# Optimization experiments

Hardware: AMD Instinct MI355X
Metric: run time of the kernel (lower is better)

Reference implementation:

```python
import jax, jax.numpy as jnp
import numpy as np

E, H, W = 1024, 16, 256  # embed_dim, num_heads, window_size
D = E // H               # head_dim


def _rmsnorm(t, w):
    eps = jnp.finfo(t.dtype).eps
    return t * jax.lax.rsqrt(jnp.mean(t * t, axis=-1, keepdims=True) + eps) * w


def setup_inputs() -> dict:
    key = jax.random.key(0)
    ks = jax.random.split(key, 11)
    B, T = 2, 2048
    s = 1.0 / np.sqrt(E)
    return {
        "x": jax.random.normal(ks[0], (B, T, E), jnp.float32),
        "wq": jax.random.normal(ks[1], (E, E), jnp.float32) * s,
        "bq": jnp.zeros((E,), jnp.float32),
        "wk": jax.random.normal(ks[2], (E, E), jnp.float32) * s,
        "bk": jnp.zeros((E,), jnp.float32),
        "wv": jax.random.normal(ks[3], (E, E), jnp.float32) * s,
        "bv": jnp.zeros((E,), jnp.float32),
        "wo": jax.random.normal(ks[4], (E, E), jnp.float32) * s,
        "bo": jnp.zeros((E,), jnp.float32),
        "qn_w": jnp.ones((D,), jnp.float32),
        "kn_w": jnp.ones((D,), jnp.float32),
    }


def reference(x, wq, bq, wk, bk, wv, bv, wo, bo, qn_w, kn_w):
    B, T, _ = x.shape
    # projections; weights stored (in, out)
    q = (x @ wq + bq).reshape(B, T, H, D).transpose(0, 2, 1, 3)  # [B,H,T,D]
    k = (x @ wk + bk).reshape(B, T, H, D).transpose(0, 2, 1, 3)
    v = (x @ wv + bv).reshape(B, T, H, D).transpose(0, 2, 1, 3)
    q = _rmsnorm(q, qn_w)
    k = _rmsnorm(k, kn_w)

    scores = jnp.einsum("bhqd,bhkd->bhqk", q, k) / jnp.sqrt(jnp.float32(D))
    row = jnp.arange(T)[:, None]
    col = jnp.arange(T)[None, :]
    invalid = (col > row) | (row - col >= W)  # causal + sliding window
    neg_inf = jnp.float32(-jnp.inf)
    scores = jnp.where(invalid, neg_inf, scores)

    # genetic fitness reweighting
    masked_attn = jnp.where(invalid, 0.0, jax.nn.softmax(scores, axis=-1))
    gene_means = jnp.mean(jax.nn.sigmoid(masked_attn), axis=-1)  # [B,H,T]
    denom = gene_means + 0.5
    sum_inv = jnp.sum(1.0 / denom, axis=2, keepdims=True)        # [B,H,1]
    fitness = 1.0 / (denom * sum_inv)                            # [B,H,T]
    scores = scores + jnp.log(fitness)[..., None]

    attn = jax.nn.softmax(scores, axis=-1)
    out = jnp.einsum("bhqk,bhkd->bhqd", attn, v)
    out = out.transpose(0, 2, 1, 3).reshape(B, T, E)
    return out @ wo + bo
```

## Files before the change

### kernel.cpp

```cpp
#include <hip/hip_runtime.h>

typedef _Float16 f16;
typedef _Float16 f16x4 __attribute__((ext_vector_type(4)));
typedef _Float16 f16x8 __attribute__((ext_vector_type(8)));
typedef float f32x4 __attribute__((ext_vector_type(4)));

#define MFMA16(a, b, c) __builtin_amdgcn_mfma_f32_16x16x32_f16(a, b, c, 0, 0, 0)

constexpr int T = 2048;
constexpr int E = 1024;
constexpr int H = 16;
constexpr int D = 64;
constexpr int WIN = 256;
#define NEGF (-1e30f)
#define L2E 1.4426950408889634f

__device__ __forceinline__ void gload16(const f16* g, f16* l) {
  __builtin_amdgcn_global_load_lds(
      (__attribute__((address_space(1))) void*)(void*)g,
      (__attribute__((address_space(3))) void*)(void*)l, 16, 0, 0);
}

__global__ __launch_bounds__(256) void cast_x_kernel(const float* __restrict__ x,
                                                     f16* __restrict__ xb) {
  int idx = (blockIdx.x * 256 + threadIdx.x) * 4;
  float4 v = *(const float4*)(x + idx);
  f16x4 o = {(f16)v.x, (f16)v.y, (f16)v.z, (f16)v.w};
  *(f16x4*)(xb + idx) = o;
}

__global__ __launch_bounds__(256) void transpose_w_kernel(
    const float* __restrict__ w0, const float* __restrict__ w1,
    const float* __restrict__ w2, const float* __restrict__ w3,
    f16* __restrict__ o0, f16* __restrict__ o1, f16* __restrict__ o2,
    f16* __restrict__ o3) {
  int z = blockIdx.z;
  const float* w = z == 0 ? w0 : z == 1 ? w1 : z == 2 ? w2 : w3;
  f16* o = z == 0 ? o0 : z == 1 ? o1 : z == 2 ? o2 : o3;
  __shared__ float tile[64][65];
  int k0 = blockIdx.x * 64, n0 = blockIdx.y * 64;
  int r = threadIdx.x >> 2, cb = (threadIdx.x & 3) * 16;
  const float* src = w + (size_t)(k0 + r) * E + n0 + cb;
#pragma unroll
  for (int j = 0; j < 16; j += 4) {
    float4 v = *(const float4*)(src + j);
    tile[r][cb + j] = v.x;
    tile[r][cb + j + 1] = v.y;
    tile[r][cb + j + 2] = v.z;
    tile[r][cb + j + 3] = v.w;
  }
  __syncthreads();
  f16 tmp[16];
#pragma unroll
  for (int j = 0; j < 16; ++j) tmp[j] = (f16)tile[cb + j][r];
  f16* dst = o + (size_t)(n0 + r) * E + k0 + cb;
  *(f16x8*)dst = *(f16x8*)&tmp[0];
  *(f16x8*)(dst + 8) = *(f16x8*)&tmp[8];
}

template <int QKV>
__global__ __launch_bounds__(256) void gemm_bt_kernel(
    const f16* __restrict__ A, const f16* __restrict__ B0,
    const f16* __restrict__ B1, const f16* __restrict__ B2,
    const float* __restrict__ c0, const float* __restrict__ c1,
    const float* __restrict__ c2, const float* __restrict__ qnw,
    const float* __restrict__ knw, f16* __restrict__ oq, f16* __restrict__ ok,
    f16* __restrict__ Vt, float* __restrict__ of32, int M, int N, int K) {
  int z = blockIdx.z;
  const f16* Bt = z == 0 ? B0 : z == 1 ? B1 : B2;
  const float* bias = z == 0 ? c0 : z == 1 ? c1 : c2;

  __shared__ f16 lA[2][8192];
  __shared__ f16 lB[2][8192];

  int m0 = blockIdx.x * 128, n0 = blockIdx.y * 128;
  int tid = threadIdx.x;
  int wid = tid >> 6, lane = tid & 63;
  int wm = wid >> 1, wn = wid & 1;
  int lr = lane & 15, lg = lane >> 4;

  f32x4 zero = {0.f, 0.f, 0.f, 0.f};
  f32x4 acc[4][4];
  for (int a = 0; a < 4; ++a)
    for (int b = 0; b < 4; ++b) acc[a][b] = zero;

  int srow = lane >> 3;
  int scol = (lane & 7) << 3;

  auto stage = [&](int buf, int k0) {
#pragma unroll
    for (int p = 0; p < 4; ++p) {
      int cc = (wid << 2) + p;
      int row = (cc << 3) + srow;
      int gc = scol ^ ((row & 7) << 3);
      gload16(A + (size_t)(m0 + row) * K + k0 + gc, &lA[buf][cc << 9]);
      gload16(Bt + (size_t)(n0 + row) * K + k0 + gc, &lB[buf][cc << 9]);
    }
  };

  int nit = K >> 6;
  stage(0, 0);
  __syncthreads();
  int cur = 0;
  for (int t = 0; t < nit; ++t) {
    if (t + 1 < nit) stage(cur ^ 1, (t + 1) << 6);
#pragma unroll
    for (int kk = 0; kk < 2; ++kk) {
      int kc = kk * 32 + (lg << 3);
      f16x8 af[4], bf[4];
#pragma unroll
      for (int mt = 0; mt < 4; ++mt) {
        int row = wm * 64 + mt * 16 + lr;
        af[mt] = *(const f16x8*)&lA[cur][((row << 6) + kc) ^ ((row & 7) << 3)];
      }
#pragma unroll
      for (int nt = 0; nt < 4; ++nt) {
        int row = wn * 64 + nt * 16 + lr;
        bf[nt] = *(const f16x8*)&lB[cur][((row << 6) + kc) ^ ((row & 7) << 3)];
      }
#pragma unroll
      for (int mt = 0; mt < 4; ++mt)
#pragma unroll
        for (int nt = 0; nt < 4; ++nt)
          acc[mt][nt] = MFMA16(af[mt], bf[nt], acc[mt][nt]);
    }
    if (t + 1 < nit) {
      __syncthreads();
      cur ^= 1;
    }
  }

  if constexpr (QKV == 1) {
    if (z < 2) {
      const float* nw = z == 0 ? qnw : knw;
      f16* o = z == 0 ? oq : ok;
      const float eps = 1.1920929e-7f;
      float wv_[4];
#pragma unroll
      for (int nt = 0; nt < 4; ++nt) wv_[nt] = nw[nt * 16 + lr];
#pragma unroll
      for (int mt = 0; mt < 4; ++mt) {
        float vbuf[4][4];
        float ss[4] = {0.f, 0.f, 0.f, 0.f};
#pragma unroll
        for (int nt = 0; nt < 4; ++nt) {
          float bv = bias[n0 + wn * 64 + nt * 16 + lr];
#pragma unroll
          for (int i = 0; i < 4; ++i) {
            float v = acc[mt][nt][i] + bv;
            vbuf[nt][i] = v;
            ss[i] += v * v;
          }
        }
        float rr[4];
#pragma unroll
        for (int i = 0; i < 4; ++i) {
          ss[i] += __shfl_xor(ss[i], 1);
          ss[i] += __shfl_xor(ss[i], 2);
          ss[i] += __shfl_xor(ss[i], 4);
          ss[i] += __shfl_xor(ss[i], 8);
          rr[i] = rsqrtf(ss[i] * (1.0f / 64.0f) + eps);
        }
        int row = m0 + wm * 64 + mt * 16 + (lg << 2);
#pragma unroll
        for (int nt = 0; nt < 4; ++nt) {
          int col = n0 + wn * 64 + nt * 16 + lr;
#pragma unroll
          for (int i = 0; i < 4; ++i)
            o[(size_t)(row + i) * N + col] = (f16)(vbuf[nt][i] * rr[i] * wv_[nt]);
        }
      }
    } else {
#pragma unroll
      for (int mt = 0; mt < 4; ++mt) {
        int row = m0 + wm * 64 + mt * 16 + (lg << 2);
        int b = row >> 11;
        int t = row & (T - 1);
#pragma unroll
        for (int nt = 0; nt < 4; ++nt) {
          int col = n0 + wn * 64 + nt * 16 + lr;
          float bv = bias[col];
          int h = col >> 6, d = col & 63;
          f16x4 pk = {(f16)(acc[mt][nt][0] + bv), (f16)(acc[mt][nt][1] + bv),
                      (f16)(acc[mt][nt][2] + bv), (f16)(acc[mt][nt][3] + bv)};
          *(f16x4*)&Vt[(((size_t)(b * H + h) * D + d) << 11) + t] = pk;
        }
      }
    }
  } else {
#pragma unroll
    for (int mt = 0; mt < 4; ++mt) {
#pragma unroll
      for (int nt = 0; nt < 4; ++nt) {
        int row = m0 + wm * 64 + mt * 16 + (lg << 2);
        int col = n0 + wn * 64 + nt * 16 + lr;
        float bv = bias[col];
#pragma unroll
        for (int i = 0; i < 4; ++i)
          of32[(size_t)(row + i) * N + col] = acc[mt][nt][i] + bv;
      }
    }
  }
}

__global__ __launch_bounds__(256) void attn_kernel(const f16* __restrict__ qn,
                                                   const f16* __restrict__ kn,
                                                   const f16* __restrict__ Vt,
                                                   f16* __restrict__ aout) {
  int q0 = blockIdx.x * 64;
  int bh = blockIdx.y;
  int b = bh >> 4, h = bh & 15;
  int tid = threadIdx.x;
  int w = tid >> 6, lane = tid & 63;
  int lr = lane & 15, lg = lane >> 4;

  __shared__ f16 lK[2][4096];
  __shared__ f16 lV[2][4096];
  __shared__ f16 lP[4096];

  const f16* Qb = qn + (size_t)(b * T + q0 + w * 16 + lr) * E + h * 64 + (lg << 3);
  f16x8 qf0 = *(const f16x8*)Qb;
  f16x8 qf1 = *(const f16x8*)(Qb + 32);

  f32x4 zero = {0.f, 0.f, 0.f, 0.f};
  f32x4 acc[4] = {zero, zero, zero, zero};
  float m[4] = {NEGF, NEGF, NEGF, NEGF};
  float l[4] = {0.f, 0.f, 0.f, 0.f};

  int mi = q0 >> 6;
  int kts = mi - 4 < 0 ? 0 : mi - 4;

  const f16* Kbase = kn + (size_t)b * T * E + h * 64;
  const f16* Vbase = Vt + (size_t)bh * D * T;

  int srow = lane >> 3;
  int scol = (lane & 7) << 3;

  auto stageKV = [&](int buf, int kt) {
    int k0 = kt << 6;
#pragma unroll
    for (int p = 0; p < 2; ++p) {
      int cc = (w << 1) + p;
      int row = (cc << 3) + srow;
      int gc = scol ^ ((row & 7) << 3);
      gload16(Kbase + (size_t)(k0 + row) * E + gc, &lK[buf][cc << 9]);
      gload16(Vbase + (size_t)row * T + k0 + gc, &lV[buf][cc << 9]);
    }
  };

  stageKV(0, kts);
  __syncthreads();
  int cur = 0;

  for (int kt = kts; kt <= mi; ++kt) {
    if (kt < mi) stageKV(cur ^ 1, kt + 1);
    int k0 = kt << 6;

    f32x4 s[4];
#pragma unroll
    for (int ct = 0; ct < 4; ++ct) s[ct] = zero;
#pragma unroll
    for (int kk = 0; kk < 2; ++kk) {
      int kc = kk * 32 + (lg << 3);
#pragma unroll
      for (int ct = 0; ct < 4; ++ct) {
        int row = ct * 16 + lr;
        f16x8 bf = *(const f16x8*)&lK[cur][((row << 6) + kc) ^ ((row & 7) << 3)];
        s[ct] = MFMA16(kk == 0 ? qf0 : qf1, bf, s[ct]);
      }
    }

    float tm[4] = {NEGF, NEGF, NEGF, NEGF};
    int rowg0 = q0 + w * 16 + (lg << 2);
#pragma unroll
    for (int ct = 0; ct < 4; ++ct) {
      int col = k0 + ct * 16 + lr;
#pragma unroll
      for (int i = 0; i < 4; ++i) {
        int rowg = rowg0 + i;
        float v = s[ct][i] * 0.125f;
        if (col > rowg || rowg - col >= WIN) v = NEGF;
        s[ct][i] = v;
        tm[i] = fmaxf(tm[i], v);
      }
    }
#pragma unroll
    for (int i = 0; i < 4; ++i) {
      tm[i] = fmaxf(tm[i], __shfl_xor(tm[i], 1));
      tm[i] = fmaxf(tm[i], __shfl_xor(tm[i], 2));
      tm[i] = fmaxf(tm[i], __shfl_xor(tm[i], 4));
      tm[i] = fmaxf(tm[i], __shfl_xor(tm[i], 8));
    }
    float fac[4], ps[4];
#pragma unroll
    for (int i = 0; i < 4; ++i) {
      float mn = fmaxf(m[i], tm[i]);
      fac[i] = exp2f((m[i] - mn) * L2E);
      m[i] = mn;
      ps[i] = 0.f;
    }
#pragma unroll
    for (int ct = 0; ct < 4; ++ct)
#pragma unroll
      for (int i = 0; i < 4; ++i) {
        float p = exp2f((s[ct][i] - m[i]) * L2E);
        s[ct][i] = p;
        ps[i] += p;
      }
#pragma unroll
    for (int i = 0; i < 4; ++i) {
      ps[i] += __shfl_xor(ps[i], 1);
      ps[i] += __shfl_xor(ps[i], 2);
      ps[i] += __shfl_xor(ps[i], 4);
      ps[i] += __shfl_xor(ps[i], 8);
      l[i] = l[i] * fac[i] + ps[i];
    }
#pragma unroll
    for (int dt = 0; dt < 4; ++dt)
#pragma unroll
      for (int i = 0; i < 4; ++i) acc[dt][i] *= fac[i];

#pragma unroll
    for (int ct = 0; ct < 4; ++ct)
#pragma unroll
      for (int i = 0; i < 4; ++i) {
        int qloc = (lg << 2) + i;
        int el = (qloc << 6) + ct * 16 + lr;
        lP[w * 1024 + (el ^ ((qloc & 7) << 3))] = (f16)s[ct][i];
      }

#pragma unroll
    for (int kk = 0; kk < 2; ++kk) {
      int kc = kk * 32 + (lg << 3);
      int ep = w * 1024 + (((lr << 6) + kc) ^ ((lr & 7) << 3));
      f16x8 pf = *(const f16x8*)&lP[ep];
#pragma unroll
      for (int dt = 0; dt < 4; ++dt) {
        int row = dt * 16 + lr;
        f16x8 vf = *(const f16x8*)&lV[cur][((row << 6) + kc) ^ ((row & 7) << 3)];
        acc[dt] = MFMA16(pf, vf, acc[dt]);
      }
    }

    if (kt < mi) {
      __syncthreads();
      cur ^= 1;
    }
  }

#pragma unroll
  for (int i = 0; i < 4; ++i) {
    float inv = 1.0f / l[i];
    int tok = q0 + w * 16 + (lg << 2) + i;
    f16* dst = aout + (size_t)(b * T + tok) * E + h * 64 + lr;
#pragma unroll
    for (int dt = 0; dt < 4; ++dt) dst[dt * 16] = (f16)(acc[dt][i] * inv);
  }
}

extern "C" void kernel_launch(void* const* d_in, const int* in_sizes, int n_in,
                              void* d_out, int out_size, void* d_ws,
                              size_t ws_size, hipStream_t stream) {
  const float* x = (const float*)d_in[0];
  const float* wq = (const float*)d_in[1];
  const float* bq = (const float*)d_in[2];
  const float* wk = (const float*)d_in[3];
  const float* bk = (const float*)d_in[4];
  const float* wv = (const float*)d_in[5];
  const float* bv = (const float*)d_in[6];
  const float* wo = (const float*)d_in[7];
  const float* bo = (const float*)d_in[8];
  const float* qn_w = (const float*)d_in[9];
  const float* kn_w = (const float*)d_in[10];
  float* out = (float*)d_out;

  char* ws = (char*)d_ws;
  const size_t MB = 1u << 20;
  f16* xb = (f16*)(ws);
  f16* wqT = (f16*)(ws + 8 * MB);
  f16* wkT = (f16*)(ws + 10 * MB);
  f16* wvT = (f16*)(ws + 12 * MB);
  f16* woT = (f16*)(ws + 14 * MB);
  f16* qn = (f16*)(ws + 16 * MB);
  f16* kn = (f16*)(ws + 24 * MB);
  f16* Vt = (f16*)(ws + 32 * MB);
  f16* aout = (f16*)(ws + 40 * MB);

  cast_x_kernel<<<4096, 256, 0, stream>>>(x, xb);
  transpose_w_kernel<<<dim3(16, 16, 4), 256, 0, stream>>>(wq, wk, wv, wo, wqT,
                                                          wkT, wvT, woT);
  gemm_bt_kernel<1><<<dim3(32, 8, 3), 256, 0, stream>>>(
      xb, wqT, wkT, wvT, bq, bk, bv, qn_w, kn_w, qn, kn, Vt, nullptr, 4096,
      1024, 1024);
  attn_kernel<<<dim3(32, 32), 256, 0, stream>>>(qn, kn, Vt, aout);
  gemm_bt_kernel<0><<<dim3(32, 8, 1), 256, 0, stream>>>(
      aout, woT, woT, woT, bo, bo, bo, nullptr, nullptr, nullptr, nullptr,
      nullptr, out, 4096, 1024, 1024);
}
```

Baseline: 106.6 us.

## Triple-buffer GEMM loads, fold Q scale into norm, skip redundant masking and rescale

The projection GEMM goes from double to triple buffering. It issues loads two stages ahead and replaces __syncthreads with explicit vmcnt waits plus raw barriers, so global loads overlap more compute. The 1/sqrt(D) scale moves into the Q RMSNorm weight, which removes a multiply per score. Attention now applies the causal/window mask only on the diagonal and window-edge tiles, and skips the online-softmax rescale when no row max grows. The cost is more LDS per GEMM block, which may lower occupancy, and the mask-skip logic depends on correct tile indexing.

```diff
diff --git a/kernel.cpp b/kernel.cpp
--- a/kernel.cpp
+++ b/kernel.cpp
@@ -70,8 +70,8 @@
   const f16* Bt = z == 0 ? B0 : z == 1 ? B1 : B2;
   const float* bias = z == 0 ? c0 : z == 1 ? c1 : c2;
 
-  __shared__ f16 lA[2][8192];
-  __shared__ f16 lB[2][8192];
+  __shared__ f16 lA[3][8192];
+  __shared__ f16 lB[3][8192];
 
   int m0 = blockIdx.x * 128, n0 = blockIdx.y * 128;
   int tid = threadIdx.x;
@@ -100,10 +100,14 @@
 
   int nit = K >> 6;
   stage(0, 0);
-  __syncthreads();
+  stage(1, 64);
+  asm volatile("s_waitcnt vmcnt(8)" ::: "memory");
+  __builtin_amdgcn_s_barrier();
+  __builtin_amdgcn_sched_barrier(0);
+
   int cur = 0;
   for (int t = 0; t < nit; ++t) {
-    if (t + 1 < nit) stage(cur ^ 1, (t + 1) << 6);
+    if (t + 2 < nit) stage(cur == 0 ? 2 : cur - 1, (t + 2) << 6);
 #pragma unroll
     for (int kk = 0; kk < 2; ++kk) {
       int kc = kk * 32 + (lg << 3);
@@ -125,8 +129,14 @@
           acc[mt][nt] = MFMA16(af[mt], bf[nt], acc[mt][nt]);
     }
     if (t + 1 < nit) {
-      __syncthreads();
-      cur ^= 1;
+      if (t + 2 < nit) {
+        asm volatile("s_waitcnt vmcnt(8)" ::: "memory");
+      } else {
+        asm volatile("s_waitcnt vmcnt(0)" ::: "memory");
+      }
+      __builtin_amdgcn_s_barrier();
+      __builtin_amdgcn_sched_barrier(0);
+      cur = (cur == 2) ? 0 : cur + 1;
     }
   }
 
@@ -135,9 +145,10 @@
       const float* nw = z == 0 ? qnw : knw;
       f16* o = z == 0 ? oq : ok;
       const float eps = 1.1920929e-7f;
+      const float osc = z == 0 ? 0.125f : 1.0f;
       float wv_[4];
 #pragma unroll
-      for (int nt = 0; nt < 4; ++nt) wv_[nt] = nw[nt * 16 + lr];
+      for (int nt = 0; nt < 4; ++nt) wv_[nt] = nw[nt * 16 + lr] * osc;
 #pragma unroll
       for (int mt = 0; mt < 4; ++mt) {
         float vbuf[4][4];
@@ -272,17 +283,25 @@
 
     float tm[4] = {NEGF, NEGF, NEGF, NEGF};
     int rowg0 = q0 + w * 16 + (lg << 2);
-#pragma unroll
-    for (int ct = 0; ct < 4; ++ct) {
-      int col = k0 + ct * 16 + lr;
-#pragma unroll
-      for (int i = 0; i < 4; ++i) {
-        int rowg = rowg0 + i;
-        float v = s[ct][i] * 0.125f;
-        if (col > rowg || rowg - col >= WIN) v = NEGF;
-        s[ct][i] = v;
-        tm[i] = fmaxf(tm[i], v);
-      }
+    bool needmask = (kt == mi) || (mi >= 4 && kt == kts);
+    if (needmask) {
+#pragma unroll
+      for (int ct = 0; ct < 4; ++ct) {
+        int col = k0 + ct * 16 + lr;
+#pragma unroll
+        for (int i = 0; i < 4; ++i) {
+          int rowg = rowg0 + i;
+          float v = s[ct][i];
+          if (col > rowg || rowg - col >= WIN) v = NEGF;
+          s[ct][i] = v;
+          tm[i] = fmaxf(tm[i], v);
+        }
+      }
+    } else {
+#pragma unroll
+      for (int ct = 0; ct < 4; ++ct)
+#pragma unroll
+        for (int i = 0; i < 4; ++i) tm[i] = fmaxf(tm[i], s[ct][i]);
     }
 #pragma unroll
     for (int i = 0; i < 4; ++i) {
@@ -291,14 +310,23 @@
       tm[i] = fmaxf(tm[i], __shfl_xor(tm[i], 4));
       tm[i] = fmaxf(tm[i], __shfl_xor(tm[i], 8));
     }
-    float fac[4], ps[4];
-#pragma unroll
-    for (int i = 0; i < 4; ++i) {
-      float mn = fmaxf(m[i], tm[i]);
-      fac[i] = exp2f((m[i] - mn) * L2E);
-      m[i] = mn;
-      ps[i] = 0.f;
-    }
+    bool up = (tm[0] > m[0]) || (tm[1] > m[1]) || (tm[2] > m[2]) ||
+              (tm[3] > m[3]);
+    if (__any(up)) {
+      float fac[4];
+#pragma unroll
+      for (int i = 0; i < 4; ++i) {
+        float mn = fmaxf(m[i], tm[i]);
+        fac[i] = exp2f((m[i] - mn) * L2E);
+        m[i] = mn;
+        l[i] *= fac[i];
+      }
+#pragma unroll
+      for (int dt = 0; dt < 4; ++dt)
+#pragma unroll
+        for (int i = 0; i < 4; ++i) acc[dt][i] *= fac[i];
+    }
+    float ps[4] = {0.f, 0.f, 0.f, 0.f};
 #pragma unroll
     for (int ct = 0; ct < 4; ++ct)
 #pragma unroll
@@ -313,12 +341,8 @@
       ps[i] += __shfl_xor(ps[i], 2);
       ps[i] += __shfl_xor(ps[i], 4);
       ps[i] += __shfl_xor(ps[i], 8);
-      l[i] = l[i] * fac[i] + ps[i];
-    }
-#pragma unroll
-    for (int dt = 0; dt < 4; ++dt)
-#pragma unroll
-      for (int i = 0; i < 4; ++i) acc[dt][i] *= fac[i];
+      l[i] += ps[i];
+    }
 
 #pragma unroll
     for (int ct = 0; ct < 4; ++ct)
```

Measured after the change: 121.7 us. +14.2%, slower.
